# Kernel tuning notes

Hardware: AMD Instinct MI355X
Metric: run time of the kernel (lower is better)

## Reference

```python
import jax, jax.numpy as jnp
import numpy as np
from jax import lax

DN = ('NCDHW', 'OIDHW', 'NCDHW')

def conv3d(x, w, b, stride, pad):
    y = lax.conv_general_dilated(x, w, (stride,) * 3, [(pad, pad)] * 3,
                                 dimension_numbers=DN)
    return y + b[None, :, None, None, None]

def conv_transpose3d(x, w, b, stride=2, pad=1):
    # torch ConvTranspose3d weight layout: (Cin, Cout, k, k, k).
    # Equivalent conv: flip spatial dims, swap in/out, lhs_dilation=stride,
    # padding = k - 1 - pad.
    k = w.shape[2]
    wf = jnp.flip(w, (2, 3, 4)).transpose(1, 0, 2, 3, 4)
    p = k - 1 - pad
    y = lax.conv_general_dilated(x, wf, (1, 1, 1), [(p, p)] * 3,
                                 lhs_dilation=(stride,) * 3,
                                 dimension_numbers=DN)
    return y + b[None, :, None, None, None]

def setup_inputs() -> dict:
    key = jax.random.key(0)
    ks = jax.random.split(key, 20)
    B, C, S = 2, 3, 64
    CD, K = 256, 1024  # codebook_dim, codebook_size

    def w(k, shape):
        fan_in = int(np.prod(shape[1:]))
        return (jax.random.normal(k, shape, jnp.float32) / np.sqrt(fan_in)).astype(jnp.float32)

    inp = {"x": jax.random.normal(ks[0], (B, C, S, S, S), jnp.float32)}
    # encoder
    inp["enc_w1"] = w(ks[1], (64, C, 4, 4, 4));   inp["enc_b1"] = jnp.zeros((64,), jnp.float32)
    inp["enc_w2"] = w(ks[2], (128, 64, 4, 4, 4)); inp["enc_b2"] = jnp.zeros((128,), jnp.float32)
    inp["enc_w3"] = w(ks[3], (256, 128, 4, 4, 4)); inp["enc_b3"] = jnp.zeros((256,), jnp.float32)
    inp["enc_w4"] = w(ks[4], (CD, 256, 1, 1, 1)); inp["enc_b4"] = jnp.zeros((CD,), jnp.float32)
    # codebook (nn.Embedding weight)
    inp["codebook"] = jax.random.normal(ks[5], (K, CD), jnp.float32)
    # decoder (ConvTranspose weights in torch (Cin, Cout, k, k, k) layout)
    inp["dec_w1"] = w(ks[6], (CD, 256, 4, 4, 4)); inp["dec_b1"] = jnp.zeros((256,), jnp.float32)
    inp["dec_w2"] = w(ks[7], (256, 128, 4, 4, 4)); inp["dec_b2"] = jnp.zeros((128,), jnp.float32)
    inp["dec_w3"] = w(ks[8], (128, 64, 4, 4, 4)); inp["dec_b3"] = jnp.zeros((64,), jnp.float32)
    inp["dec_w4"] = w(ks[9], (C, 64, 4, 4, 4));   inp["dec_b4"] = jnp.zeros((C,), jnp.float32)
    return inp

def reference(x, enc_w1, enc_b1, enc_w2, enc_b2, enc_w3, enc_b3, enc_w4, enc_b4,
              codebook, dec_w1, dec_b1, dec_w2, dec_b2, dec_w3, dec_b3, dec_w4, dec_b4):
    # encoder
    h = jax.nn.relu(conv3d(x, enc_w1, enc_b1, 2, 1))
    h = jax.nn.relu(conv3d(h, enc_w2, enc_b2, 2, 1))
    h = jax.nn.relu(conv3d(h, enc_w3, enc_b3, 2, 1))
    latent = conv3d(h, enc_w4, enc_b4, 1, 0)  # (B, CD, H, W, D)
    B = latent.shape[0]
    H, W, D = latent.shape[2], latent.shape[3], latent.shape[4]
    CD = codebook.shape[1]
    # Faithful to torch: raw row-major .view(B, -1, CD) on channel-first latent
    lat = latent.reshape(B, -1, CD)  # (B, N, CD), N = H*W*D
    # argmin of L2 norm == argmin of squared distance (expand-norm trick,
    # avoids materializing the (B,N,K,CD) broadcast tensor)
    d2 = ((lat * lat).sum(-1, keepdims=True)
          - 2.0 * jnp.einsum('bnd,kd->bnk', lat, codebook)
          + (codebook * codebook).sum(-1)[None, None, :])  # (B, N, K)
    quantized_idx = jnp.argmin(d2, axis=-1)  # (B, N)
    quantized = codebook[quantized_idx]      # (B, N, CD)
    q = quantized.reshape(B, H, W, D, CD).transpose(0, 4, 1, 2, 3)  # (B, CD, H, W, D)
    # decoder
    h = jax.nn.relu(conv_transpose3d(q, dec_w1, dec_b1))
    h = jax.nn.relu(conv_transpose3d(h, dec_w2, dec_b2))
    h = jax.nn.relu(conv_transpose3d(h, dec_w3, dec_b3))
    reconstructed = jnp.tanh(conv3d(h, dec_w4, dec_b4, 1, 0))  # (B, C, S-3, S-3, S-3)
    return reconstructed, quantized_idx
```

## Files before the change

kernel.cpp:

```cpp
#include <hip/hip_runtime.h>
#include <cfloat>
#include <cmath>


using f32x4  = __attribute__((ext_vector_type(4))) float;
using bf16x8 = __attribute__((ext_vector_type(8))) short;
typedef float f32x4u __attribute__((ext_vector_type(4), aligned(4)));
typedef unsigned short u16x4u __attribute__((ext_vector_type(4), aligned(4)));

__device__ __forceinline__ unsigned short f32_to_bf16(float f) {
    unsigned int u = __float_as_uint(f);
    u += 0x7fffu + ((u >> 16) & 1u);
    return (unsigned short)(u >> 16);
}
__device__ __forceinline__ void split_bf16(float v, unsigned short& h, unsigned short& l) {
    h = f32_to_bf16(v);
    float hf = __uint_as_float((unsigned)h << 16);
    l = f32_to_bf16(v - hf);
}
__device__ __forceinline__ void store_act(float* p, float v) { *p = v; }
__device__ __forceinline__ void store_act(unsigned short* p, float v) { *p = f32_to_bf16(v); }

template <typename V>
__device__ __forceinline__ bf16x8 pack_b(V r0, V r1) {
    bf16x8 b;
    b[0] = (short)r0[0]; b[1] = (short)r0[1]; b[2] = (short)r0[2]; b[3] = (short)r0[3];
    b[4] = (short)r1[0]; b[5] = (short)r1[1]; b[6] = (short)r1[2]; b[7] = (short)r1[3];
    return b;
}

__global__ __launch_bounds__(256)
void prep_split_w(const float* __restrict__ w, short* __restrict__ whi,
                  short* __restrict__ wlo, long total)
{
    long idx = (long)blockIdx.x * blockDim.x + threadIdx.x;
    if (idx >= total) return;
    unsigned short h, l;
    split_bf16(w[idx], h, l);
    whi[idx] = (short)h; wlo[idx] = (short)l;
}

__global__ __launch_bounds__(256)
void prep_split_w_frag(const float* __restrict__ w, short* __restrict__ whi,
                       short* __restrict__ wlo, int CIN, int COUT)
{
    const int K = CIN * 64;
    const int MT = COUT >> 4;
    long total = (long)COUT * K;
    long idx = (long)blockIdx.x * blockDim.x + threadIdx.x;
    if (idx >= total) return;
    int kk = (int)(idx & 7); long r = idx >> 3;
    int l  = (int)(r & 63);  r >>= 6;
    int m  = (int)(r % MT);
    int s  = (int)(r / MT);
    int n16 = l & 15, quad = l >> 4;
    int co = m * 16 + n16;
    int korig = s * 32 + quad * 8 + kk;
    unsigned short h, lo16;
    split_bf16(w[(long)co * K + korig], h, lo16);
    whi[idx] = (short)h; wlo[idx] = (short)lo16;
}

__global__ __launch_bounds__(256)
void pad_input_split(const float* __restrict__ x, unsigned short* __restrict__ xhi,
                     unsigned short* __restrict__ xlo)
{
    const int D = 64, PD = 66, PRX = 68, BC = 6;
    long total = (long)BC * PD * PD * PRX;
    long idx = (long)blockIdx.x * blockDim.x + threadIdx.x;
    if (idx >= total) return;
    int px = (int)(idx % PRX); long t = idx / PRX;
    int py = (int)(t % PD); t /= PD;
    int pz = (int)(t % PD); int c = (int)(t / PD);
    int ix = px - 1, iy = py - 1, iz = pz - 1;
    float v = 0.0f;
    if ((unsigned)ix < (unsigned)D && (unsigned)iy < (unsigned)D && (unsigned)iz < (unsigned)D)
        v = x[(((long)c * D + iz) * D + iy) * D + ix];
    unsigned short h, l;
    split_bf16(v, h, l);
    xhi[idx] = h; xlo[idx] = l;
}

__global__ __launch_bounds__(256)
void zero_halo_ps(unsigned short* __restrict__ p, int C, int PD, int PRX)
{
    long total = (long)C * PD * PD * PRX;
    long idx = (long)blockIdx.x * blockDim.x + threadIdx.x;
    if (idx >= total) return;
    int px = (int)(idx % PRX); long t = idx / PRX;
    int py = (int)(t % PD); t /= PD;
    int pz = (int)(t % PD);
    if (px == 0 || px >= PD - 1 || py == 0 || py == PD - 1 || pz == 0 || pz == PD - 1)
        p[idx] = 0;
}

template <typename T>
__global__ __launch_bounds__(256) void zero_halo_t(T* __restrict__ p, int C, int PD)
{
    long total = (long)C * PD * PD * PD;
    long idx = (long)blockIdx.x * blockDim.x + threadIdx.x;
    if (idx >= total) return;
    int px = (int)(idx % PD); long t = idx / PD;
    int py = (int)(t % PD); t /= PD;
    int pz = (int)(t % PD);
    if (px == 0 || px == PD - 1 || py == 0 || py == PD - 1 || pz == 0 || pz == PD - 1)
        p[idx] = (T)0;
}

template <int CIN, int COUT, int DOUT, int PD, int PRX, int MTW, int OWT,
          int OWHALF, int KSPLIT, int OUTSPLIT>
__global__ __launch_bounds__(256)
void conv_s2_mfma(const unsigned short* __restrict__ xhi,
                  const unsigned short* __restrict__ xlo,
                  const short* __restrict__ Whi, const short* __restrict__ Wlo,
                  const float* __restrict__ bias,
                  unsigned short* __restrict__ yhi, unsigned short* __restrict__ ylo,
                  float* __restrict__ yf,
                  int OPD, int OPRX, int po, long sstride)
{
    constexpr int K = CIN * 64;
    constexpr int MWAVES = COUT / (16 * MTW);
    constexpr int RPB = 4 / MWAVES;
    constexpr int KN = (CIN * 2) / KSPLIT;

    int bx = blockIdx.x;
    const int ks = (KSPLIT > 1) ? (bx % KSPLIT) : 0;
    const int rowblk = (KSPLIT > 1) ? (bx / KSPLIT) : bx;
    const int lane = (int)threadIdx.x & 63, w = (int)threadIdx.x >> 6;
    const int mi = (MWAVES == 4) ? w : 0;
    const int ri = (MWAVES == 4) ? 0 : w;
    const int rowid = rowblk * RPB + ri;
    const int n16 = lane & 15, quad = lane >> 4;

    int b, od, oh, ow;
    if (OWHALF) {
        constexpr int NOH = DOUT / 2;
        const int ohb = rowid % NOH; int t = rowid / NOH;
        od = t % DOUT; b = t / DOUT;
        oh = ohb * 2 + (n16 >> 3);
        ow = n16 & 7;
    } else {
        const int owt = rowid % OWT; int t = rowid / OWT;
        oh = t % DOUT; t /= DOUT;
        od = t % DOUT; b = t / DOUT;
        ow = owt * 16 + n16;
    }

    const int co0 = mi * (MTW * 16);

    f32x4 acc[MTW];
    #pragma unroll
    for (int mt = 0; mt < MTW; ++mt)
        #pragma unroll
        for (int r = 0; r < 4; ++r) {
            int co = co0 + mt * 16 + quad * 4 + r;
            acc[mt][r] = (ks == 0) ? bias[co] : 0.0f;
        }

    const int sg0 = ks * KN;
    const long chs = (long)PD * PD * PRX;
    long off = ((long)(b * CIN + (sg0 >> 1)) * PD + (2 * od + (quad >> 1))) * PD * PRX
             + (long)(2 * oh + (quad & 1) * 2) * PRX + 2 * ow;
    const unsigned short* phi = xhi + off;
    const unsigned short* plo = xlo + off;
    const long incA = 2L * PD * PRX;
    const long incB = chs - 2L * PD * PRX;

    const short* a0h = Whi + (long)(co0 + n16) * K + sg0 * 32 + quad * 8;
    const short* a0l = Wlo + (long)(co0 + n16) * K + sg0 * 32 + quad * 8;

    #pragma unroll 2
    for (int s = 0; s < KN; ++s) {
        u16x4u h0 = *(const u16x4u*)phi;
        u16x4u h1 = *(const u16x4u*)(phi + PRX);
        u16x4u l0 = *(const u16x4u*)plo;
        u16x4u l1 = *(const u16x4u*)(plo + PRX);
        bf16x8 bhi = pack_b(h0, h1);
        bf16x8 blo = pack_b(l0, l1);
        #pragma unroll
        for (int mt = 0; mt < MTW; ++mt) {
            bf16x8 ah = *(const bf16x8*)(a0h + (long)mt * 16 * K + s * 32);
            bf16x8 al = *(const bf16x8*)(a0l + (long)mt * 16 * K + s * 32);
            acc[mt] = __builtin_amdgcn_mfma_f32_16x16x32_bf16(ah, bhi, acc[mt], 0, 0, 0);
            acc[mt] = __builtin_amdgcn_mfma_f32_16x16x32_bf16(ah, blo, acc[mt], 0, 0, 0);
            acc[mt] = __builtin_amdgcn_mfma_f32_16x16x32_bf16(al, bhi, acc[mt], 0, 0, 0);
        }
        long inc = (s & 1) ? incB : incA;
        phi += inc; plo += inc;
    }

    if (OUTSPLIT) {
        #pragma unroll
        for (int mt = 0; mt < MTW; ++mt)
            #pragma unroll
            for (int r = 0; r < 4; ++r) {
                int co = co0 + mt * 16 + quad * 4 + r;
                float v = fmaxf(acc[mt][r], 0.0f);
                unsigned short h, l;
                split_bf16(v, h, l);
                long o = (((long)(b * COUT + co) * OPD + od + po) * OPD + oh + po) * OPRX
                       + ow + po;
                yhi[o] = h; ylo[o] = l;
            }
    } else {
        #pragma unroll
        for (int mt = 0; mt < MTW; ++mt)
            #pragma unroll
            for (int r = 0; r < 4; ++r) {
                int co = co0 + mt * 16 + quad * 4 + r;
                long o = (long)ks * sstride
                       + (((long)(b * COUT + co) * OPD + od) * OPD + oh) * OPRX + ow;
                yf[o] = acc[mt][r];
            }
    }
}

template <int CIN, int COUT, int DOUT, int PD, int PRX, int MTW, int OWT,
          int OWHALF, int KSPLIT, int OUTSPLIT>
__global__ __launch_bounds__(256)
void conv_s2_mfma_lds(const unsigned short* __restrict__ xhi,
                      const unsigned short* __restrict__ xlo,
                      const short* __restrict__ Whi, const short* __restrict__ Wlo,
                      const float* __restrict__ bias,
                      unsigned short* __restrict__ yhi, unsigned short* __restrict__ ylo,
                      float* __restrict__ yf,
                      int OPD, int OPRX, int po, long sstride)
{
    constexpr int K = CIN * 64;
    constexpr int MWAVES = COUT / (16 * MTW);
    constexpr int RPB = 4 / MWAVES;
    constexpr int KN = (CIN * 2) / KSPLIT;
    constexpr int TILE = COUT * 32;
    constexpr int PASSES = TILE / (256 * 8);
    static_assert(PASSES >= 1, "tile too small for 256-thread staging");

    int bx = blockIdx.x;
    const int ks = (KSPLIT > 1) ? (bx % KSPLIT) : 0;
    const int rowblk = (KSPLIT > 1) ? (bx / KSPLIT) : bx;
    const int tid = (int)threadIdx.x;
    const int lane = tid & 63, w = tid >> 6;
    const int mi = (MWAVES == 4) ? w : 0;
    const int ri = (MWAVES == 4) ? 0 : w;
    const int rowid = rowblk * RPB + ri;
    const int n16 = lane & 15, quad = lane >> 4;

    int b, od, oh, ow;
    if (OWHALF) {
        constexpr int NOH = DOUT / 2;
        const int ohb = rowid % NOH; int t = rowid / NOH;
        od = t % DOUT; b = t / DOUT;
        oh = ohb * 2 + (n16 >> 3);
        ow = n16 & 7;
    } else {
        const int owt = rowid % OWT; int t = rowid / OWT;
        oh = t % DOUT; t /= DOUT;
        od = t % DOUT; b = t / DOUT;
        ow = owt * 16 + n16;
    }

    const int co0 = mi * (MTW * 16);

    f32x4 acc[MTW];
    #pragma unroll
    for (int mt = 0; mt < MTW; ++mt)
        #pragma unroll
        for (int r = 0; r < 4; ++r) {
            int co = co0 + mt * 16 + quad * 4 + r;
            acc[mt][r] = (ks == 0) ? bias[co] : 0.0f;
        }

    const int sg0 = ks * KN;
    const long chs = (long)PD * PD * PRX;
    long off = ((long)(b * CIN + (sg0 >> 1)) * PD + (2 * od + (quad >> 1))) * PD * PRX
             + (long)(2 * oh + (quad & 1) * 2) * PRX + 2 * ow;
    const unsigned short* phi = xhi + off;
    const unsigned short* plo = xlo + off;
    const long incA = 2L * PD * PRX;
    const long incB = chs - 2L * PD * PRX;

    __shared__ short AhiB[2][TILE];
    __shared__ short AloB[2][TILE];

    {
        const long tb = (long)sg0 * TILE;
        #pragma unroll
        for (int j = 0; j < PASSES; ++j) {
            const int o = tid * 8 + j * 2048;
            *(bf16x8*)(&AhiB[0][o]) = *(const bf16x8*)(Whi + tb + o);
            *(bf16x8*)(&AloB[0][o]) = *(const bf16x8*)(Wlo + tb + o);
        }
    }
    __syncthreads();

    #pragma unroll 1
    for (int s = 0; s < KN; ++s) {
        const int cur = s & 1;
        const bool more = (s + 1 < KN);
        bf16x8 nh[PASSES], nl[PASSES];
        if (more) {
            const long tb = (long)(sg0 + s + 1) * TILE;
            #pragma unroll
            for (int j = 0; j < PASSES; ++j) {
                const int o = tid * 8 + j * 2048;
                nh[j] = *(const bf16x8*)(Whi + tb + o);
                nl[j] = *(const bf16x8*)(Wlo + tb + o);
            }
        }

        u16x4u h0 = *(const u16x4u*)phi;
        u16x4u h1 = *(const u16x4u*)(phi + PRX);
        u16x4u l0 = *(const u16x4u*)plo;
        u16x4u l1 = *(const u16x4u*)(plo + PRX);
        bf16x8 bhi = pack_b(h0, h1);
        bf16x8 blo = pack_b(l0, l1);

        #pragma unroll
        for (int mt = 0; mt < MTW; ++mt) {
            const int m = mi * MTW + mt;
            bf16x8 ah = *(const bf16x8*)(&AhiB[cur][(m * 64 + lane) * 8]);
            bf16x8 al = *(const bf16x8*)(&AloB[cur][(m * 64 + lane) * 8]);
            acc[mt] = __builtin_amdgcn_mfma_f32_16x16x32_bf16(ah, bhi, acc[mt], 0, 0, 0);
            acc[mt] = __builtin_amdgcn_mfma_f32_16x16x32_bf16(ah, blo, acc[mt], 0, 0, 0);
            acc[mt] = __builtin_amdgcn_mfma_f32_16x16x32_bf16(al, bhi, acc[mt], 0, 0, 0);
        }

        long inc = (s & 1) ? incB : incA;
        phi += inc; plo += inc;

        if (more) {
            #pragma unroll
            for (int j = 0; j < PASSES; ++j) {
                const int o = tid * 8 + j * 2048;
                *(bf16x8*)(&AhiB[cur ^ 1][o]) = nh[j];
                *(bf16x8*)(&AloB[cur ^ 1][o]) = nl[j];
            }
        }
        __syncthreads();
    }

    if (OUTSPLIT) {
        #pragma unroll
        for (int mt = 0; mt < MTW; ++mt)
            #pragma unroll
            for (int r = 0; r < 4; ++r) {
                int co = co0 + mt * 16 + quad * 4 + r;
                float v = fmaxf(acc[mt][r], 0.0f);
                unsigned short h, l;
                split_bf16(v, h, l);
                long o = (((long)(b * COUT + co) * OPD + od + po) * OPD + oh + po) * OPRX
                       + ow + po;
                yhi[o] = h; ylo[o] = l;
            }
    } else {
        #pragma unroll
        for (int mt = 0; mt < MTW; ++mt)
            #pragma unroll
            for (int r = 0; r < 4; ++r) {
                int co = co0 + mt * 16 + quad * 4 + r;
                long o = (long)ks * sstride
                       + (((long)(b * COUT + co) * OPD + od) * OPD + oh) * OPRX + ow;
                yf[o] = acc[mt][r];
            }
    }
}

__global__ __launch_bounds__(256)
void combine4_relu(const float* __restrict__ p, float* __restrict__ y, long N, long ss)
{
    long idx = (long)blockIdx.x * blockDim.x + threadIdx.x;
    if (idx >= N) return;
    float v = p[idx] + p[idx + ss] + p[idx + 2 * ss] + p[idx + 3 * ss];
    y[idx] = fmaxf(v, 0.0f);
}

__global__ __launch_bounds__(128)
void conv1x1_b(const float* __restrict__ x, const float* __restrict__ w,
               const float* __restrict__ bias, float* __restrict__ y)
{
    const int co = blockIdx.x & 255, b = blockIdx.x >> 8;
    const int s4 = (int)threadIdx.x * 4;
    const float* xb = x + (long)b * 256 * 512 + s4;
    const float* wr = w + (long)co * 256;
    float bv = bias[co];
    float4 acc = {bv, bv, bv, bv};
    for (int ci = 0; ci < 256; ++ci) {
        float wv = wr[ci];
        float4 xv = *(const float4*)(xb + (long)ci * 512);
        acc.x = fmaf(xv.x, wv, acc.x); acc.y = fmaf(xv.y, wv, acc.y);
        acc.z = fmaf(xv.z, wv, acc.z); acc.w = fmaf(xv.w, wv, acc.w);
    }
    *(float4*)(y + (long)(b * 256 + co) * 512 + s4) = acc;
}

__global__ void codenorm_kernel(const float* __restrict__ cb, float* __restrict__ norms)
{
    int k = blockIdx.x;
    int lane = threadIdx.x;
    float s = 0.0f;
    const float* row = cb + (long)k * 256;
    for (int d = lane; d < 256; d += 64) { float v = row[d]; s = fmaf(v, v, s); }
    for (int off = 32; off > 0; off >>= 1) s += __shfl_down(s, off);
    if (lane == 0) norms[k] = s;
}

__global__ __launch_bounds__(256)
void vq_kernel(const float* __restrict__ lat, const float* __restrict__ cb,
               const float* __restrict__ norms, unsigned short* __restrict__ q,
               float* __restrict__ idx_out)
{
    __shared__ __align__(16) float row[256];
    __shared__ float s_best[256];
    __shared__ int   s_bidx[256];
    int r = blockIdx.x;
    int t = threadIdx.x;
    row[t] = lat[(long)r * 256 + t];
    __syncthreads();

    const float4* rowv = (const float4*)row;
    float latn = 0.0f;
    #pragma unroll 4
    for (int d = 0; d < 64; ++d) {
        float4 rv = rowv[d];
        latn = fmaf(rv.x, rv.x, latn); latn = fmaf(rv.y, rv.y, latn);
        latn = fmaf(rv.z, rv.z, latn); latn = fmaf(rv.w, rv.w, latn);
    }

    float best = FLT_MAX;
    int bidx = 0x7fffffff;
    for (int j = 0; j < 4; ++j) {
        int k = t + 256 * j;
        const float4* cr = (const float4*)(cb + (long)k * 256);
        float dot = 0.0f;
        #pragma unroll 4
        for (int d = 0; d < 64; ++d) {
            float4 c = cr[d]; float4 rv = rowv[d];
            dot = fmaf(rv.x, c.x, dot); dot = fmaf(rv.y, c.y, dot);
            dot = fmaf(rv.z, c.z, dot); dot = fmaf(rv.w, c.w, dot);
        }
        float sc = latn - 2.0f * dot + norms[k];
        if (sc < best || (sc == best && k < bidx)) { best = sc; bidx = k; }
    }
    s_best[t] = best; s_bidx[t] = bidx;
    __syncthreads();
    for (int off = 128; off > 0; off >>= 1) {
        if (t < off) {
            float o = s_best[t + off]; int oi = s_bidx[t + off];
            if (o < s_best[t] || (o == s_best[t] && oi < s_bidx[t])) {
                s_best[t] = o; s_bidx[t] = oi;
            }
        }
        __syncthreads();
    }
    int bk = s_bidx[0];
    int b = r >> 9, n = r & 511;
    int zz = n >> 6, yy = (n >> 3) & 7, xx = n & 7;
    q[(long)(b * 256 + t) * 1000 + ((long)(zz + 1) * 10 + (yy + 1)) * 10 + (xx + 1)]
        = f32_to_bf16(cb[(long)bk * 256 + t]);
    if (t == 0) idx_out[r] = (float)bk;
}

__global__ __launch_bounds__(256)
void prep_convt_w(const float* __restrict__ w, short* __restrict__ Ap,
                  int Cin, int Cout, int xflip)
{
    const int K = Cin * 8;
    long total = 8L * Cout * K;
    long idx = (long)blockIdx.x * blockDim.x + threadIdx.x;
    if (idx >= total) return;
    int k = (int)(idx % K);
    int co = (int)((idx / K) % Cout);
    int p = (int)(idx / ((long)K * Cout));
    int ci = k >> 3, a = k & 7;
    int az = (a >> 2) & 1, ay = (a >> 1) & 1, ax = a & 1;
    int pz = p >> 2, py = (p >> 1) & 1, px = p & 1;
    int axw = xflip ? (1 - ax) : ax;
    int kd = (1 - pz) + 2 * az, kh = (1 - py) + 2 * ay, kw = (1 - px) + 2 * axw;
    float v = w[((long)ci * Cout + co) * 64 + kd * 16 + kh * 4 + kw];
    Ap[idx] = (short)f32_to_bf16(v);
}

__global__ __launch_bounds__(256)
void prep_convt_w_frag(const float* __restrict__ w, short* __restrict__ Ap,
                       int Cin, int Cout, int xflip)
{
    const int MG = Cout >> 6;
    const int nsteps = Cin >> 2;
    long total = 8L * MG * nsteps * 2048;
    long idx = (long)blockIdx.x * blockDim.x + threadIdx.x;
    if (idx >= total) return;
    int kk = (int)(idx & 7); long r = idx >> 3;
    int l  = (int)(r & 63);  r >>= 6;
    int cb = (int)(r & 3);   r >>= 2;
    int s  = (int)(r % nsteps); r /= nsteps;
    int mg = (int)(r % MG);
    int p  = (int)(r / MG);

    int n16 = l & 15, quad = l >> 4;
    int korig = s * 32 + quad * 8 + kk;
    int co = mg * 64 + cb * 16 + n16;
    int ci = korig >> 3, a = korig & 7;
    int az = (a >> 2) & 1, ay = (a >> 1) & 1, ax = a & 1;
    int pz = p >> 2, py = (p >> 1) & 1, px = p & 1;
    int axw = xflip ? (1 - ax) : ax;
    int kd = (1 - pz) + 2 * az, kh = (1 - py) + 2 * ay, kw = (1 - px) + 2 * axw;
    float v = w[((long)ci * Cout + co) * 64 + kd * 16 + kh * 4 + kw];
    Ap[idx] = (short)f32_to_bf16(v);
}

template <int CIN, int COUT, int DIN, int OPAD, typename OutT>
__global__ __launch_bounds__(256)
void convt_mfma(const unsigned short* __restrict__ Xp, const short* __restrict__ Ap,
                const float* __restrict__ bias, OutT* __restrict__ Y)
{
    constexpr int PD = DIN + 2;
    constexpr int PD3 = PD * PD * PD;
    constexpr int T = DIN >> 2;
    constexpr int NT = T * T * T;
    constexpr int SLAB = NT / 8;
    constexpr int OPD = 2 * DIN + 2 * OPAD;
    constexpr int K = CIN * 8;
    constexpr int MG = COUT >> 6;
    constexpr int nsteps = K >> 5;

    int bx = blockIdx.x;
    const int xcd = bx & 7;
    int local = bx >> 3;
    const int px = local & 1; local >>= 1;
    const int mg = local % MG; local /= MG;
    const int ntin = local % SLAB;
    const int pzy = local / SLAB;
    const int pz = pzy >> 1, py = pzy & 1;
    const int p = pz * 4 + py * 2 + px;
    const int nt = xcd * SLAB + ntin;

    const int lane = threadIdx.x & 63, wave = threadIdx.x >> 6;
    const int n16 = lane & 15, quad = lane >> 4;

    const int tx = nt % T, ty = (nt / T) % T, tz = nt / (T * T);
    const int mz = tz * 4 + wave, my = ty * 4 + (n16 >> 2), mx = tx * 4 + (n16 & 3);
    const int sp = ((mz + pz) * PD + (my + py)) * PD + (mx + px);

    const unsigned short* xq = Xp + (long)quad * PD3 + sp;

    const int cobase = mg * 64;
    const short* ap0 = Ap + ((long)p * COUT + cobase + n16) * K + quad * 8;

    f32x4 acc[4];
    #pragma unroll
    for (int cb = 0; cb < 4; ++cb) {
        const float* bp = bias + cobase + cb * 16 + quad * 4;
        acc[cb][0] = bp[0]; acc[cb][1] = bp[1]; acc[cb][2] = bp[2]; acc[cb][3] = bp[3];
    }

    #pragma unroll 4
    for (int s = 0; s < nsteps; ++s) {
        const unsigned short* xs = xq + (long)s * 4 * PD3;
        bf16x8 bf;
        bf[0] = (short)xs[(PD + 1) * PD + 1];
        bf[1] = (short)xs[(PD + 1) * PD];
        bf[2] = (short)xs[PD * PD + 1];
        bf[3] = (short)xs[PD * PD];
        bf[4] = (short)xs[PD + 1];
        bf[5] = (short)xs[PD];
        bf[6] = (short)xs[1];
        bf[7] = (short)xs[0];
        #pragma unroll
        for (int cb = 0; cb < 4; ++cb) {
            bf16x8 af = *(const bf16x8*)(ap0 + (long)cb * 16 * K + s * 32);
            acc[cb] = __builtin_amdgcn_mfma_f32_16x16x32_bf16(af, bf, acc[cb], 0, 0, 0);
        }
    }

    const int opz = 2 * mz + pz + OPAD, opy = 2 * my + py + OPAD, opx = 2 * mx + px + OPAD;
    const long spo = ((long)opz * OPD + opy) * OPD + opx;
    #pragma unroll
    for (int cb = 0; cb < 4; ++cb) {
        #pragma unroll
        for (int r = 0; r < 4; ++r) {
            int co = cobase + cb * 16 + quad * 4 + r;
            float v = fmaxf(acc[cb][r], 0.0f);
            store_act(Y + (long)co * OPD * OPD * OPD + spo, v);
        }
    }
}

template <int CIN, int COUT, int DIN, int OPAD, int MXP, int MYP, typename OutT>
__global__ __launch_bounds__(256)
void convt_mfma_v2(const unsigned short* __restrict__ Xp, const short* __restrict__ Ap,
                   const float* __restrict__ bias, OutT* __restrict__ Y)
{
    constexpr int PD = DIN + 2;
    constexpr int PD3 = PD * PD * PD;
    constexpr int OPD = 2 * DIN + 2 * OPAD;
    constexpr int K = CIN * 8;
    constexpr int MG = COUT >> 6;
    constexpr int nsteps = K >> 5;
    static_assert(nsteps >= 2, "need at least 2 K-steps");
    constexpr int MXT = DIN / (16 * MXP);
    constexpr int MYT = DIN / (4 * MYP);
    constexpr int MZS = DIN / 8;
    constexpr int TPE = MXP * MYP;

    int bx = blockIdx.x;
    const int xcd = bx & 7;
    int local = bx >> 3;
    const int px = local & 1; local >>= 1;
    const int py = local & 1; local >>= 1;
    const int mg = local % MG; local /= MG;
    const int mxt = local % MXT; local /= MXT;
    const int myt = local % MYT; local /= MYT;
    const int pz = local & 1; local >>= 1;
    const int mzin = local;
    const int mz = xcd * MZS + mzin;
    const int p = pz * 4 + py * 2 + px;

    const int lane = threadIdx.x & 63, wave = threadIdx.x >> 6;
    const int n16 = lane & 15, quad = lane >> 4;

    const int mx0 = mxt * (16 * MXP) + n16;
    const int my0 = myt * (4 * MYP) + wave * MYP;
    const int baseX = mx0 & ~1;
    const int sh = 16 * ((n16 & 1) + px);
    const long sp = ((long)(mz + pz) * PD + (my0 + py)) * PD + baseX;

    const unsigned short* xq = Xp + (long)quad * PD3 + sp;

    const short* ApT = Ap + (((long)p * MG + mg) * nsteps) * 2048;

    __shared__ short Abuf[2][2048];

    f32x4 acc[TPE][4];
    #pragma unroll
    for (int t = 0; t < TPE; ++t)
        #pragma unroll
        for (int cb = 0; cb < 4; ++cb) {
            const float* bp = bias + (mg * 64) + cb * 16 + quad * 4;
            acc[t][cb][0] = bp[0]; acc[t][cb][1] = bp[1];
            acc[t][cb][2] = bp[2]; acc[t][cb][3] = bp[3];
        }

    constexpr int rowoff[4] = { (PD + 1) * PD, PD * PD, PD, 0 };
    union Frag { unsigned u[4]; bf16x8 b; };

    const int chunkoff = wave * 512 + lane * 8;

    {
        bf16x8 a0 = *(const bf16x8*)(ApT + chunkoff);
        *(bf16x8*)(&Abuf[0][chunkoff]) = a0;
    }
    __syncthreads();

    #pragma unroll 1
    for (int s = 0; s < nsteps; ++s) {
        const int cur = s & 1;
        bf16x8 anext;
        const bool more = (s + 1 < nsteps);
        if (more)
            anext = *(const bf16x8*)(ApT + (long)(s + 1) * 2048 + chunkoff);

        const unsigned short* xs = xq + (long)s * 4 * PD3;
        unsigned long long xr[TPE][4];
        #pragma unroll
        for (int t = 0; t < TPE; ++t) {
            const int toff = (MXP > 1) ? t * 16 : t * PD;
            #pragma unroll
            for (int j = 0; j < 4; ++j) {
                union { u16x4u v; unsigned long long u; } ld;
                ld.v = *(const u16x4u*)(xs + toff + rowoff[j]);
                xr[t][j] = ld.u;
            }
        }

        bf16x8 af[4];
        #pragma unroll
        for (int cb = 0; cb < 4; ++cb)
            af[cb] = *(const bf16x8*)(&Abuf[cur][cb * 512 + lane * 8]);

        #pragma unroll
        for (int t = 0; t < TPE; ++t) {
            Frag fr;
            #pragma unroll
            for (int j = 0; j < 4; ++j)
                fr.u[j] = (unsigned)(xr[t][j] >> sh);
            #pragma unroll
            for (int cb = 0; cb < 4; ++cb)
                acc[t][cb] = __builtin_amdgcn_mfma_f32_16x16x32_bf16(af[cb], fr.b,
                                                                     acc[t][cb], 0, 0, 0);
        }

        if (more)
            *(bf16x8*)(&Abuf[cur ^ 1][chunkoff]) = anext;
        __syncthreads();
    }

    const int opz = 2 * mz + pz + OPAD;
    #pragma unroll
    for (int t = 0; t < TPE; ++t) {
        const int opx = 2 * (mx0 + ((MXP > 1) ? t * 16 : 0)) + px + OPAD;
        const int opy = 2 * (my0 + ((MYP > 1) ? t : 0)) + py + OPAD;
        const long spo = ((long)opz * OPD + opy) * OPD + opx;
        #pragma unroll
        for (int cb = 0; cb < 4; ++cb) {
            #pragma unroll
            for (int r = 0; r < 4; ++r) {
                int co = (mg * 64) + cb * 16 + quad * 4 + r;
                float v = fmaxf(acc[t][cb][r], 0.0f);
                store_act(Y + (long)co * OPD * OPD * OPD + spo, v);
            }
        }
    }
}

__global__ __launch_bounds__(256)
void prep_dec4A_frag(const float* __restrict__ w, short* __restrict__ Aw)
{
    int idx = blockIdx.x * 256 + (int)threadIdx.x;
    int kk = idx & 7;
    int l  = (idx >> 3) & 63;
    int s  = idx >> 9;
    int n16 = l & 15, quad = l >> 4;
    int k = s * 32 + quad * 8 + kk;
    float v = (n16 < 3) ? w[n16 * 4096 + k] : 0.0f;
    Aw[idx] = (short)f32_to_bf16(v);
}

__global__ __launch_bounds__(256)
void conv_dec4_mfma(const float* __restrict__ d3, const short* __restrict__ Aw,
                    const float* __restrict__ bias, float* __restrict__ y)
{
    constexpr int D = 64, Dout = 61;
    int bx = blockIdx.x;
    const int slab = bx & 7;
    const int i = bx >> 3;
    const int od = slab * 8 + (i >> 4);
    const int oh0 = (i & 15) * 4;
    if (od >= Dout) return;
    const int tid = (int)threadIdx.x;
    const int lane = tid & 63, wave = tid >> 6;
    const int n16 = lane & 15, quad = lane >> 4;
    const int ow = wave * 16 + n16;

    __shared__ float Xs[2][2][7][68];

    f32x4 acc[4];
    #pragma unroll
    for (int j = 0; j < 4; ++j)
        #pragma unroll
        for (int r = 0; r < 4; ++r) {
            int co = quad * 4 + r;
            acc[j][r] = (co < 3) ? bias[co] : 0.0f;
        }

    const int kd0 = quad >> 1;
    const int kh0 = (quad & 1) * 2;

    const int srow = tid >> 4;
    const int sseg = tid & 15;
    const int szi = srow / 7, syi = srow % 7;
    const bool sact = (srow < 14);
    const long sbase = (((long)(od + szi) * D) + min(oh0 + syi, D - 1)) * D + sseg * 4;
    auto saddr = [&](int s) {
        return d3 + sbase + ((long)((s >> 1) * D + (s & 1) * 2)) * D * D;
    };

    if (sact)
        *(f32x4u*)(&Xs[0][szi][syi][sseg * 4]) = *(const f32x4u*)saddr(0);
    __syncthreads();

    #pragma unroll 1
    for (int s = 0; s < 128; ++s) {
        const int cur = s & 1;
        const bool more = (s + 1 < 128);
        f32x4u nv;
        if (more && sact)
            nv = *(const f32x4u*)saddr(s + 1);

        bf16x8 af = *(const bf16x8*)(Aw + ((long)s * 64 + lane) * 8);

        unsigned p0[5], p1[5];
        #pragma unroll
        for (int r = 0; r < 5; ++r) {
            f32x4u v = *(const f32x4u*)(&Xs[cur][kd0][kh0 + r][ow]);
            p0[r] = (__float_as_uint(v[0]) >> 16) | (__float_as_uint(v[1]) & 0xffff0000u);
            p1[r] = (__float_as_uint(v[2]) >> 16) | (__float_as_uint(v[3]) & 0xffff0000u);
        }
        #pragma unroll
        for (int j = 0; j < 4; ++j) {
            union { unsigned u[4]; bf16x8 b; } fr;
            fr.u[0] = p0[j];     fr.u[1] = p1[j];
            fr.u[2] = p0[j + 1]; fr.u[3] = p1[j + 1];
            acc[j] = __builtin_amdgcn_mfma_f32_16x16x32_bf16(af, fr.b, acc[j], 0, 0, 0);
        }

        if (more && sact)
            *(f32x4u*)(&Xs[cur ^ 1][szi][syi][sseg * 4]) = nv;
        __syncthreads();
    }

    if (ow < Dout && quad == 0) {
        #pragma unroll
        for (int j = 0; j < 4; ++j) {
            const int oh = oh0 + j;
            if (oh >= Dout) continue;
            #pragma unroll
            for (int r = 0; r < 3; ++r)
                y[((long)(r * Dout + od) * Dout + oh) * Dout + ow] = tanhf(acc[j][r]);
        }
    }
}

extern "C" void kernel_launch(void* const* d_in, const int* in_sizes, int n_in,
                              void* d_out, int out_size, void* d_ws, size_t ws_size,
                              hipStream_t stream)
{
    const float* x        = (const float*)d_in[0];
    const float* enc_w1   = (const float*)d_in[1];
    const float* enc_b1   = (const float*)d_in[2];
    const float* enc_w2   = (const float*)d_in[3];
    const float* enc_b2   = (const float*)d_in[4];
    const float* enc_w3   = (const float*)d_in[5];
    const float* enc_b3   = (const float*)d_in[6];
    const float* enc_w4   = (const float*)d_in[7];
    const float* enc_b4   = (const float*)d_in[8];
    const float* codebook = (const float*)d_in[9];
    const float* dec_w1   = (const float*)d_in[10];
    const float* dec_b1   = (const float*)d_in[11];
    const float* dec_w2   = (const float*)d_in[12];
    const float* dec_b2   = (const float*)d_in[13];
    const float* dec_w3   = (const float*)d_in[14];
    const float* dec_b3   = (const float*)d_in[15];
    const float* dec_w4   = (const float*)d_in[16];
    const float* dec_b4   = (const float*)d_in[17];

    float* out = (float*)d_out;
    float* idx_out = out + 2L * 3 * 61 * 61 * 61;

    char* wsb = (char*)d_ws;
    float*          cn   = (float*)wsb;
    unsigned short* qp   = (unsigned short*)(wsb + 4096);
    short*          Ap1  = (short*)(wsb + 1028096);
    short*          Ap2  = (short*)(wsb + 9416704);
    short*          Ap3  = (short*)(wsb + 13611008);
    short*          Aw4  = (short*)(wsb + 14659584);
    short*          W1hi = (short*)(wsb + 14790656);
    short*          W1lo = (short*)(wsb + 14815232);
    short*          W2hi = (short*)(wsb + 14839808);
    short*          W2lo = (short*)(wsb + 15888384);
    short*          W3hi = (short*)(wsb + 16936960);
    short*          W3lo = (short*)(wsb + 21131264);
    char* arena = wsb + 25325568;
    unsigned short* xphi = (unsigned short*)arena;
    unsigned short* xplo = (unsigned short*)(arena + 3554496);
    unsigned short* h1hi = (unsigned short*)(arena + 7108992);
    unsigned short* h1lo = (unsigned short*)(arena + 17762688);
    unsigned short* h2hi = (unsigned short*)(arena + 28416384);
    unsigned short* h2lo = (unsigned short*)(arena + 31734144);
    float*          pp3  = (float*)(arena + 35051904);
    float*          h3   = (float*)(arena + 39246208);
    float*          lat  = (float*)(arena + 40294784);
    unsigned short* d1 = (unsigned short*)arena;
    unsigned short* d2 = (unsigned short*)(arena + 2985984);
    float*          d3 = (float*)(arena + 13047808);

    dim3 blk(256);
    auto nblk = [](long n) { return dim3((unsigned)((n + 255) / 256)); };

    prep_convt_w<<<nblk(8L * 256 * 2048), blk, 0, stream>>>(dec_w1, Ap1, 256, 256, 0);
    prep_convt_w_frag<<<nblk(8L * 128 * 2048), blk, 0, stream>>>(dec_w2, Ap2, 256, 128, 1);
    prep_convt_w_frag<<<nblk(8L * 64 * 1024), blk, 0, stream>>>(dec_w3, Ap3, 128, 64, 1);
    prep_dec4A_frag<<<dim3(256), blk, 0, stream>>>(dec_w4, Aw4);
    prep_split_w<<<nblk(12288), blk, 0, stream>>>(enc_w1, W1hi, W1lo, 12288);
    prep_split_w_frag<<<nblk(524288), blk, 0, stream>>>(enc_w2, W2hi, W2lo, 64, 128);
    prep_split_w_frag<<<nblk(2097152), blk, 0, stream>>>(enc_w3, W3hi, W3lo, 128, 256);

    pad_input_split<<<nblk(6L * 66 * 66 * 68), blk, 0, stream>>>(x, xphi, xplo);
    zero_halo_ps<<<nblk(128L * 34 * 34 * 36), blk, 0, stream>>>(h1hi, 128, 34, 36);
    zero_halo_ps<<<nblk(128L * 34 * 34 * 36), blk, 0, stream>>>(h1lo, 128, 34, 36);
    conv_s2_mfma<3, 64, 32, 66, 68, 4, 2, 0, 1, 1><<<dim3(1024), blk, 0, stream>>>(
        xphi, xplo, W1hi, W1lo, enc_b1, h1hi, h1lo, nullptr, 34, 36, 1, 0);
    zero_halo_ps<<<nblk(256L * 18 * 18 * 20), blk, 0, stream>>>(h2hi, 256, 18, 20);
    zero_halo_ps<<<nblk(256L * 18 * 18 * 20), blk, 0, stream>>>(h2lo, 256, 18, 20);
    conv_s2_mfma_lds<64, 128, 16, 34, 36, 2, 1, 0, 1, 1><<<dim3(512), blk, 0, stream>>>(
        h1hi, h1lo, W2hi, W2lo, enc_b2, h2hi, h2lo, nullptr, 18, 20, 1, 0);
    conv_s2_mfma_lds<128, 256, 8, 18, 20, 4, 1, 1, 4, 0><<<dim3(256), blk, 0, stream>>>(
        h2hi, h2lo, W3hi, W3lo, enc_b3, nullptr, nullptr, pp3, 8, 8, 0, 262144);
    combine4_relu<<<nblk(262144), blk, 0, stream>>>(pp3, h3, 262144, 262144);
    conv1x1_b<<<dim3(512), dim3(128), 0, stream>>>(h3, enc_w4, enc_b4, lat);

    codenorm_kernel<<<dim3(1024), dim3(64), 0, stream>>>(codebook, cn);
    zero_halo_t<unsigned short><<<nblk(512L * 10 * 10 * 10), blk, 0, stream>>>(qp, 512, 10);
    vq_kernel<<<dim3(1024), blk, 0, stream>>>(lat, codebook, cn, qp, idx_out);

    zero_halo_t<unsigned short><<<nblk(256L * 18 * 18 * 18), blk, 0, stream>>>(d1, 256, 18);
    zero_halo_t<unsigned short><<<nblk(128L * 34 * 34 * 34), blk, 0, stream>>>(d2, 128, 34);

    for (int b = 0; b < 2; ++b) {
        const unsigned short* qb = qp + (long)b * 256 * 1000;
        float* outb = out + (long)b * 3 * 226981;
        convt_mfma<256, 256, 8, 1, unsigned short><<<dim3(256), blk, 0, stream>>>(
            qb, Ap1, dec_b1, d1);
        convt_mfma_v2<256, 128, 16, 1, 1, 2, unsigned short><<<dim3(512), blk, 0, stream>>>(
            d1, Ap2, dec_b2, d2);
        convt_mfma_v2<128, 64, 32, 0, 2, 1, float><<<dim3(2048), blk, 0, stream>>>(
            d2, Ap3, dec_b3, d3);
        conv_dec4_mfma<<<dim3(8 * 8 * 16), blk, 0, stream>>>(d3, Aw4, dec_b4, outb);
    }
}
```

Baseline: 1.062 ms.

## Transpose codebook and process four latent rows per VQ block for reuse

Adds a kernel that transposes the codebook so consecutive threads read contiguous columns (coalesced float4 loads), and rewrites the VQ kernel so each block handles four latent rows, with each thread computing a 4x4 register tile of dot products. This targets the uncoalesced strided codebook reads and the repeated streaming of the full codebook once per latent row in the old kernel. It adds an extra transpose launch and workspace buffer, cuts the grid from 1024 to 256 blocks, and raises register use.

```diff
diff --git a/kernel.cpp b/kernel.cpp
--- a/kernel.cpp
+++ b/kernel.cpp
@@ -404,59 +404,101 @@
 }
 
 __global__ __launch_bounds__(256)
-void vq_kernel(const float* __restrict__ lat, const float* __restrict__ cb,
-               const float* __restrict__ norms, unsigned short* __restrict__ q,
-               float* __restrict__ idx_out)
-{
-    __shared__ __align__(16) float row[256];
-    __shared__ float s_best[256];
-    __shared__ int   s_bidx[256];
-    int r = blockIdx.x;
-    int t = threadIdx.x;
-    row[t] = lat[(long)r * 256 + t];
+void transpose_cb(const float* __restrict__ cb, float* __restrict__ cbT)
+{
+    int idx = blockIdx.x * 256 + (int)threadIdx.x;
+    int d = idx & 255, k = idx >> 8;
+    cbT[(long)d * 1024 + k] = cb[(long)k * 256 + d];
+}
+
+__global__ __launch_bounds__(256)
+void vq_kernel4(const float* __restrict__ lat, const float* __restrict__ cb,
+                const float* __restrict__ cbT, const float* __restrict__ norms,
+                unsigned short* __restrict__ q, float* __restrict__ idx_out)
+{
+    __shared__ __align__(16) float rows[4][256];
+    __shared__ float s_best[4][256];
+    __shared__ int   s_bidx[4][256];
+    const int r0 = blockIdx.x * 4;
+    const int t = (int)threadIdx.x;
+
+    #pragma unroll
+    for (int j = 0; j < 4; ++j)
+        rows[j][t] = lat[(long)(r0 + j) * 256 + t];
     __syncthreads();
 
-    const float4* rowv = (const float4*)row;
-    float latn = 0.0f;
-    #pragma unroll 4
-    for (int d = 0; d < 64; ++d) {
-        float4 rv = rowv[d];
-        latn = fmaf(rv.x, rv.x, latn); latn = fmaf(rv.y, rv.y, latn);
-        latn = fmaf(rv.z, rv.z, latn); latn = fmaf(rv.w, rv.w, latn);
-    }
-
-    float best = FLT_MAX;
-    int bidx = 0x7fffffff;
+    float latn[4];
+    #pragma unroll
     for (int j = 0; j < 4; ++j) {
-        int k = t + 256 * j;
-        const float4* cr = (const float4*)(cb + (long)k * 256);
-        float dot = 0.0f;
+        const float4* rowv = (const float4*)rows[j];
+        float a = 0.0f;
         #pragma unroll 4
         for (int d = 0; d < 64; ++d) {
-            float4 c = cr[d]; float4 rv = rowv[d];
-            dot = fmaf(rv.x, c.x, dot); dot = fmaf(rv.y, c.y, dot);
-            dot = fmaf(rv.z, c.z, dot); dot = fmaf(rv.w, c.w, dot);
-        }
-        float sc = latn - 2.0f * dot + norms[k];
-        if (sc < best || (sc == best && k < bidx)) { best = sc; bidx = k; }
-    }
-    s_best[t] = best; s_bidx[t] = bidx;
+            float4 rv = rowv[d];
+            a = fmaf(rv.x, rv.x, a); a = fmaf(rv.y, rv.y, a);
+            a = fmaf(rv.z, rv.z, a); a = fmaf(rv.w, rv.w, a);
+        }
+        latn[j] = a;
+    }
+
+    float dot[4][4] = {};
+    const float* ct = cbT + t * 4;
+    #pragma unroll 4
+    for (int d = 0; d < 256; ++d) {
+        float4 c4 = *(const float4*)(ct + (long)d * 1024);
+        #pragma unroll
+        for (int j = 0; j < 4; ++j) {
+            float rv = rows[j][d];
+            dot[j][0] = fmaf(rv, c4.x, dot[j][0]);
+            dot[j][1] = fmaf(rv, c4.y, dot[j][1]);
+            dot[j][2] = fmaf(rv, c4.z, dot[j][2]);
+            dot[j][3] = fmaf(rv, c4.w, dot[j][3]);
+        }
+    }
+
+    float4 nv = *(const float4*)(norms + t * 4);
+    float nr[4] = {nv.x, nv.y, nv.z, nv.w};
+
+    #pragma unroll
+    for (int j = 0; j < 4; ++j) {
+        float best = FLT_MAX;
+        int bidx = 0x7fffffff;
+        #pragma unroll
+        for (int c = 0; c < 4; ++c) {
+            float sc = latn[j] - 2.0f * dot[j][c] + nr[c];
+            int k = t * 4 + c;
+            if (sc < best || (sc == best && k < bidx)) { best = sc; bidx = k; }
+        }
+        s_best[j][t] = best; s_bidx[j][t] = bidx;
+    }
     __syncthreads();
     for (int off = 128; off > 0; off >>= 1) {
         if (t < off) {
-            float o = s_best[t + off]; int oi = s_bidx[t + off];
-            if (o < s_best[t] || (o == s_best[t] && oi < s_bidx[t])) {
-                s_best[t] = o; s_bidx[t] = oi;
+            #pragma unroll
+            for (int j = 0; j < 4; ++j) {
+                float o = s_best[j][t + off]; int oi = s_bidx[j][t + off];
+                if (o < s_best[j][t] || (o == s_best[j][t] && oi < s_bidx[j][t])) {
+                    s_best[j][t] = o; s_bidx[j][t] = oi;
+                }
             }
         }
         __syncthreads();
     }
-    int bk = s_bidx[0];
-    int b = r >> 9, n = r & 511;
-    int zz = n >> 6, yy = (n >> 3) & 7, xx = n & 7;
-    q[(long)(b * 256 + t) * 1000 + ((long)(zz + 1) * 10 + (yy + 1)) * 10 + (xx + 1)]
-        = f32_to_bf16(cb[(long)bk * 256 + t]);
-    if (t == 0) idx_out[r] = (float)bk;
+
+    #pragma unroll
+    for (int j = 0; j < 4; ++j) {
+        const int bk = s_bidx[j][0];
+        const int r = r0 + j;
+        const int b = r >> 9, n = r & 511;
+        const int zz = n >> 6, yy = (n >> 3) & 7, xx = n & 7;
+        q[(long)(b * 256 + t) * 1000 + ((long)(zz + 1) * 10 + (yy + 1)) * 10 + (xx + 1)]
+            = f32_to_bf16(cb[(long)bk * 256 + t]);
+    }
+    if (t == 0) {
+        #pragma unroll
+        for (int j = 0; j < 4; ++j)
+            idx_out[r0 + j] = (float)s_bidx[j][0];
+    }
 }
 
 __global__ __launch_bounds__(256)
@@ -861,6 +903,7 @@
     unsigned short* d1 = (unsigned short*)arena;
     unsigned short* d2 = (unsigned short*)(arena + 2985984);
     float*          d3 = (float*)(arena + 13047808);
+    float*          cbT = (float*)(wsb + 105482240);
 
     dim3 blk(256);
     auto nblk = [](long n) { return dim3((unsigned)((n + 255) / 256)); };
@@ -872,6 +915,7 @@
     prep_split_w<<<nblk(12288), blk, 0, stream>>>(enc_w1, W1hi, W1lo, 12288);
     prep_split_w_frag<<<nblk(524288), blk, 0, stream>>>(enc_w2, W2hi, W2lo, 64, 128);
     prep_split_w_frag<<<nblk(2097152), blk, 0, stream>>>(enc_w3, W3hi, W3lo, 128, 256);
+    transpose_cb<<<dim3(1024), blk, 0, stream>>>(codebook, cbT);
 
     pad_input_split<<<nblk(6L * 66 * 66 * 68), blk, 0, stream>>>(x, xphi, xplo);
     zero_halo_ps<<<nblk(128L * 34 * 34 * 36), blk, 0, stream>>>(h1hi, 128, 34, 36);
@@ -889,7 +933,7 @@
 
     codenorm_kernel<<<dim3(1024), dim3(64), 0, stream>>>(codebook, cn);
     zero_halo_t<unsigned short><<<nblk(512L * 10 * 10 * 10), blk, 0, stream>>>(qp, 512, 10);
-    vq_kernel<<<dim3(1024), blk, 0, stream>>>(lat, codebook, cn, qp, idx_out);
+    vq_kernel4<<<dim3(256), blk, 0, stream>>>(lat, codebook, cbT, cn, qp, idx_out);
 
     zero_halo_t<unsigned short><<<nblk(256L * 18 * 18 * 18), blk, 0, stream>>>(d1, 256, 18);
     zero_halo_t<unsigned short><<<nblk(128L * 34 * 34 * 34), blk, 0, stream>>>(d2, 128, 34);
```

Result: faster. 985.7 us (-7.2%).
